# Optimization experiments

Measured on AMD Instinct MI355X. Metric: run time of the kernel, lower is better.

## Reference

```python
import jax, jax.numpy as jnp
import numpy as np

DIM = 1024
N_HEADS = 16
HEAD_DIM = DIM // N_HEADS
FF_DIM = 4096
EPS = 1e-8


def rms_norm(x, scale):
    # norm = ||x||_2 * d^{-1/2}; out = scale * x / (norm + eps)
    norm = jnp.linalg.norm(x, axis=-1, keepdims=True) * (x.shape[-1] ** -0.5)
    return scale * x / (norm + EPS)


def rope_cos_sin(seq_len, dtype=jnp.float32):
    # inv_freq over even indices of head_dim; after the truncation branch in
    # apply_rotary_pos_emb, effective cos/sin have size head_dim//2.
    inv_freq = 1.0 / (10000.0 ** (jnp.arange(0, HEAD_DIM, 2, dtype=jnp.float32) / HEAD_DIM))
    t = jnp.arange(seq_len, dtype=jnp.float32)
    freqs = t[:, None] * inv_freq[None, :]  # [S, head_dim//2]
    return jnp.cos(freqs).astype(dtype), jnp.sin(freqs).astype(dtype)


def apply_rope(x, cos, sin):
    # x: [B, S, H, hd]; cos/sin: [S, hd//2] broadcast over batch and heads
    c = cos[None, :, None, :]
    s = sin[None, :, None, :]
    x1, x2 = jnp.split(x, 2, axis=-1)
    return jnp.concatenate([x1 * c - x2 * s, x1 * s + x2 * c], axis=-1)


def setup_inputs() -> dict:
    key = jax.random.key(0)
    ks = jax.random.split(key, 10)
    B, S = 2, 2048
    std = DIM ** -0.5
    inp = {
        "x": jax.random.normal(ks[0], (B, S, DIM), jnp.float32),
        "mask": jnp.tril(jnp.ones((S, S), dtype=bool)),
        "qkv_w": jax.random.normal(ks[1], (3 * DIM, DIM), jnp.float32) * std,
        "attn_out_w": jax.random.normal(ks[2], (DIM, DIM), jnp.float32) * std,
        "gate_w": jax.random.normal(ks[3], (FF_DIM, DIM), jnp.float32) * std,
        "gate_b": jnp.zeros((FF_DIM,), jnp.float32),
        "lin_w": jax.random.normal(ks[4], (FF_DIM, DIM), jnp.float32) * std,
        "lin_b": jnp.zeros((FF_DIM,), jnp.float32),
        "ff_out_w": jax.random.normal(ks[5], (DIM, FF_DIM), jnp.float32) * (FF_DIM ** -0.5),
        "norm1_scale": jnp.ones((DIM,), jnp.float32),
        "norm2_scale": jnp.ones((DIM,), jnp.float32),
    }
    return inp


def reference(x, mask, qkv_w, attn_out_w, gate_w, gate_b, lin_w, lin_b,
              ff_out_w, norm1_scale, norm2_scale):
    B, S, _ = x.shape
    residual = x
    qkv = (x @ qkv_w.T).reshape(B, S, 3, N_HEADS, HEAD_DIM)
    q, k, v = qkv[:, :, 0], qkv[:, :, 1], qkv[:, :, 2]  # [B,S,H,hd]
    cos, sin = rope_cos_sin(S, x.dtype)
    q = apply_rope(q, cos, sin)
    k = apply_rope(k, cos, sin)
    # naive full attention, materializing [B,H,S,S] as the source does
    scores = jnp.einsum('bqhd,bkhd->bhqk', q, k) / jnp.sqrt(jnp.asarray(HEAD_DIM, x.dtype))
    scores = jnp.where(mask[None, None, :, :], scores, jnp.asarray(-1e9, x.dtype))
    attn = jax.nn.softmax(scores, axis=-1)
    out = jnp.einsum('bhqk,bkhd->bqhd', attn, v).reshape(B, S, DIM)
    out = out @ attn_out_w.T
    x = rms_norm(residual + out, norm1_scale)
    residual = x
    ff = jax.nn.sigmoid(x @ gate_w.T + gate_b) * (x @ lin_w.T + lin_b)
    ff = ff @ ff_out_w.T
    x = rms_norm(residual + ff, norm2_scale)
    return x
```

## Files before the change

kernel.cpp:

```cpp
#include <hip/hip_runtime.h>
#include <hip/hip_bf16.h>
#include <math.h>

#define DIMSZ 1024
#define NHEAD 16
#define HDIM 64
#define FFDIM 4096
#define SEQ 2048
#define NBATCH 2

typedef unsigned short ushortt;
typedef __attribute__((ext_vector_type(8))) short frag8;
typedef __attribute__((ext_vector_type(4))) float f32x4;

__device__ __forceinline__ float u2f(ushortt u) {
  return __uint_as_float(((unsigned)u) << 16);
}
__device__ __forceinline__ ushortt f2bu(float f) {
  unsigned x = __float_as_uint(f);
  return (ushortt)((x + 0x7FFFu + ((x >> 16) & 1u)) >> 16);
}

__global__ __launch_bounds__(256) void cast_f2b(
    const float* __restrict__ src, ushortt* __restrict__ dst, int n) {
  int i = (blockIdx.x * 256 + threadIdx.x) * 4;
  if (i >= n) return;
  float4 f = *(const float4*)(src + i);
  ushort4 u;
  u.x = f2bu(f.x); u.y = f2bu(f.y); u.z = f2bu(f.z); u.w = f2bu(f.w);
  *(ushort4*)(dst + i) = u;
}

template <int EPI>
__global__ __launch_bounds__(256) void gemm_mfma(
    const ushortt* __restrict__ A, const ushortt* __restrict__ W,
    void* __restrict__ Cv, int M, int N, int K) {
  __shared__ __align__(16) short As[2][128 * 32];
  __shared__ __align__(16) short Bs[2][128 * 32];
  const int tid = threadIdx.x;
  const int wave = tid >> 6;
  const int lane = tid & 63;
  const int bm = blockIdx.y * 128;
  const int bn = blockIdx.x * 128;
  const int wm = (wave >> 1) * 64;
  const int wn = (wave & 1) * 64;

  f32x4 acc[4][4] = {};

  const int sr = lane >> 2;
  const int sc = (lane & 3) * 8;
  const ushortt* pa0 = A + (size_t)(bm + wave * 16 + sr) * K + sc;
  const ushortt* pa1 = pa0 + (size_t)64 * K;
  const ushortt* pb0 = W + (size_t)(bn + wave * 16 + sr) * K + sc;
  const ushortt* pb1 = pb0 + (size_t)64 * K;
  const int lo0 = (wave * 16) * 32;
  const int lo1 = (64 + wave * 16) * 32;

  const int fr = lane & 15;
  const int fq = (lane >> 4) * 8;
  const int nt = K >> 5;

  auto stage = [&](int t, int buf) {
    const int ko = t * 32;
    short* ab = &As[0][0] + buf * 4096;
    short* bb = &Bs[0][0] + buf * 4096;
    __builtin_amdgcn_global_load_lds(
        (const __attribute__((address_space(1))) void*)(pa0 + ko),
        (__attribute__((address_space(3))) void*)(ab + lo0), 16, 0, 0);
    __builtin_amdgcn_global_load_lds(
        (const __attribute__((address_space(1))) void*)(pa1 + ko),
        (__attribute__((address_space(3))) void*)(ab + lo1), 16, 0, 0);
    __builtin_amdgcn_global_load_lds(
        (const __attribute__((address_space(1))) void*)(pb0 + ko),
        (__attribute__((address_space(3))) void*)(bb + lo0), 16, 0, 0);
    __builtin_amdgcn_global_load_lds(
        (const __attribute__((address_space(1))) void*)(pb1 + ko),
        (__attribute__((address_space(3))) void*)(bb + lo1), 16, 0, 0);
  };

  stage(0, 0);
  __syncthreads();

  for (int t = 0; t < nt; ++t) {
    if (t + 1 < nt) stage(t + 1, (t + 1) & 1);
    const short* as = &As[0][0] + (t & 1) * 4096;
    const short* bs = &Bs[0][0] + (t & 1) * 4096;

    frag8 af[4], bf[4];
#pragma unroll
    for (int mi = 0; mi < 4; ++mi)
      af[mi] = *(const frag8*)&as[(wm + mi * 16 + fr) * 32 + fq];
#pragma unroll
    for (int ni = 0; ni < 4; ++ni)
      bf[ni] = *(const frag8*)&bs[(wn + ni * 16 + fr) * 32 + fq];
#pragma unroll
    for (int mi = 0; mi < 4; ++mi)
#pragma unroll
      for (int ni = 0; ni < 4; ++ni)
        acc[mi][ni] = __builtin_amdgcn_mfma_f32_16x16x32_bf16(
            af[mi], bf[ni], acc[mi][ni], 0, 0, 0);
    __syncthreads();
  }

  const int er = (lane >> 4) * 4;
  const int ec = lane & 15;
#pragma unroll
  for (int mi = 0; mi < 4; ++mi)
#pragma unroll
    for (int ni = 0; ni < 4; ++ni)
#pragma unroll
      for (int r = 0; r < 4; ++r) {
        int m = bm + wm + mi * 16 + er + r;
        int n = bn + wn + ni * 16 + ec;
        size_t o = (size_t)m * N + n;
        float v = acc[mi][ni][r];
        if (EPI == 0) {
          ((float*)Cv)[o] = v;
        } else {
          ((ushortt*)Cv)[o] = f2bu(v);
        }
      }
}

__global__ __launch_bounds__(256) void gemm_gatelin(
    const ushortt* __restrict__ A, const ushortt* __restrict__ Wg,
    const ushortt* __restrict__ Wl, ushortt* __restrict__ Cv,
    const float* __restrict__ gbias, const float* __restrict__ lbias,
    int M, int N, int K) {
  __shared__ __align__(16) short As[2][128 * 32];
  __shared__ __align__(16) short Gs[2][128 * 32];
  __shared__ __align__(16) short Ls[2][128 * 32];
  const int tid = threadIdx.x;
  const int wave = tid >> 6;
  const int lane = tid & 63;
  const int bm = blockIdx.y * 128;
  const int bn = blockIdx.x * 128;
  const int wm = (wave >> 1) * 64;
  const int wn = (wave & 1) * 64;

  f32x4 accg[4][4] = {};
  f32x4 accl[4][4] = {};

  const int sr = lane >> 2;
  const int sc = (lane & 3) * 8;
  const ushortt* pa0 = A + (size_t)(bm + wave * 16 + sr) * K + sc;
  const ushortt* pa1 = pa0 + (size_t)64 * K;
  const ushortt* pg0 = Wg + (size_t)(bn + wave * 16 + sr) * K + sc;
  const ushortt* pg1 = pg0 + (size_t)64 * K;
  const ushortt* pl0 = Wl + (size_t)(bn + wave * 16 + sr) * K + sc;
  const ushortt* pl1 = pl0 + (size_t)64 * K;
  const int lo0 = (wave * 16) * 32;
  const int lo1 = (64 + wave * 16) * 32;

  const int fr = lane & 15;
  const int fq = (lane >> 4) * 8;
  const int nt = K >> 5;

  auto stage = [&](int t, int buf) {
    const int ko = t * 32;
    short* ab = &As[0][0] + buf * 4096;
    short* gb = &Gs[0][0] + buf * 4096;
    short* lb = &Ls[0][0] + buf * 4096;
    __builtin_amdgcn_global_load_lds(
        (const __attribute__((address_space(1))) void*)(pa0 + ko),
        (__attribute__((address_space(3))) void*)(ab + lo0), 16, 0, 0);
    __builtin_amdgcn_global_load_lds(
        (const __attribute__((address_space(1))) void*)(pa1 + ko),
        (__attribute__((address_space(3))) void*)(ab + lo1), 16, 0, 0);
    __builtin_amdgcn_global_load_lds(
        (const __attribute__((address_space(1))) void*)(pg0 + ko),
        (__attribute__((address_space(3))) void*)(gb + lo0), 16, 0, 0);
    __builtin_amdgcn_global_load_lds(
        (const __attribute__((address_space(1))) void*)(pg1 + ko),
        (__attribute__((address_space(3))) void*)(gb + lo1), 16, 0, 0);
    __builtin_amdgcn_global_load_lds(
        (const __attribute__((address_space(1))) void*)(pl0 + ko),
        (__attribute__((address_space(3))) void*)(lb + lo0), 16, 0, 0);
    __builtin_amdgcn_global_load_lds(
        (const __attribute__((address_space(1))) void*)(pl1 + ko),
        (__attribute__((address_space(3))) void*)(lb + lo1), 16, 0, 0);
  };

  stage(0, 0);
  __syncthreads();

  for (int t = 0; t < nt; ++t) {
    if (t + 1 < nt) stage(t + 1, (t + 1) & 1);
    const short* as = &As[0][0] + (t & 1) * 4096;
    const short* gs = &Gs[0][0] + (t & 1) * 4096;
    const short* ls = &Ls[0][0] + (t & 1) * 4096;

    frag8 af[4], gf[4], lf[4];
#pragma unroll
    for (int mi = 0; mi < 4; ++mi)
      af[mi] = *(const frag8*)&as[(wm + mi * 16 + fr) * 32 + fq];
#pragma unroll
    for (int ni = 0; ni < 4; ++ni) {
      gf[ni] = *(const frag8*)&gs[(wn + ni * 16 + fr) * 32 + fq];
      lf[ni] = *(const frag8*)&ls[(wn + ni * 16 + fr) * 32 + fq];
    }
#pragma unroll
    for (int mi = 0; mi < 4; ++mi)
#pragma unroll
      for (int ni = 0; ni < 4; ++ni) {
        accg[mi][ni] = __builtin_amdgcn_mfma_f32_16x16x32_bf16(
            af[mi], gf[ni], accg[mi][ni], 0, 0, 0);
        accl[mi][ni] = __builtin_amdgcn_mfma_f32_16x16x32_bf16(
            af[mi], lf[ni], accl[mi][ni], 0, 0, 0);
      }
    __syncthreads();
  }

  const int er = (lane >> 4) * 4;
  const int ec = lane & 15;
#pragma unroll
  for (int mi = 0; mi < 4; ++mi)
#pragma unroll
    for (int ni = 0; ni < 4; ++ni)
#pragma unroll
      for (int r = 0; r < 4; ++r) {
        int m = bm + wm + mi * 16 + er + r;
        int n = bn + wn + ni * 16 + ec;
        size_t o = (size_t)m * N + n;
        float g = accg[mi][ni][r] + gbias[n];
        float l = accl[mi][ni][r] + lbias[n];
        float sig = 1.0f / (1.0f + __expf(-g));
        ((ushortt*)Cv)[o] = f2bu(sig * l);
      }
}

__global__ __launch_bounds__(256) void gemm_ffout(
    const ushortt* __restrict__ A, const float* __restrict__ Bw,
    float* __restrict__ C, int lda, int koff, int first) {
  __shared__ __align__(16) short As[2][128 * 32];
  __shared__ __align__(16) short Bs[2][128 * 32];
  const int tid = threadIdx.x;
  const int wave = tid >> 6;
  const int lane = tid & 63;
  const int bm = blockIdx.y * 128;
  const int bn = blockIdx.x * 128;
  const int wm = (wave >> 1) * 64;
  const int wn = (wave & 1) * 64;

  f32x4 acc[4][4] = {};

  const int sr = lane >> 2;
  const int sc = (lane & 3) * 8;
  const ushortt* pa0 = A + (size_t)(bm + wave * 16 + sr) * lda + sc;
  const ushortt* pa1 = pa0 + (size_t)64 * lda;
  const int lo0 = (wave * 16) * 32;
  const int lo1 = (64 + wave * 16) * 32;

  const int br = tid >> 2;
  const int kc = (tid & 3) * 8;
  const float* pb0 = Bw + (size_t)(bn + br) * FFDIM + koff + kc;
  const float* pb1 = pb0 + (size_t)64 * FFDIM;

  const int fr = lane & 15;
  const int fq = (lane >> 4) * 8;
  const int nt = 2048 >> 5;

  float4 f0, f1, f2, f3;
  auto bload = [&](int t) {
    const float* p0 = pb0 + t * 32;
    const float* p1 = pb1 + t * 32;
    f0 = *(const float4*)p0; f1 = *(const float4*)(p0 + 4);
    f2 = *(const float4*)p1; f3 = *(const float4*)(p1 + 4);
  };
  auto pk = [&](float4 a, float4 b) {
    frag8 v;
    v[0] = (short)f2bu(a.x); v[1] = (short)f2bu(a.y);
    v[2] = (short)f2bu(a.z); v[3] = (short)f2bu(a.w);
    v[4] = (short)f2bu(b.x); v[5] = (short)f2bu(b.y);
    v[6] = (short)f2bu(b.z); v[7] = (short)f2bu(b.w);
    return v;
  };
  auto bwrite = [&](int buf) {
    *(frag8*)&Bs[buf][tid * 8] = pk(f0, f1);
    *(frag8*)&Bs[buf][2048 + tid * 8] = pk(f2, f3);
  };
  auto astage = [&](int t, int buf) {
    const int ko = t * 32;
    short* ab = &As[0][0] + buf * 4096;
    __builtin_amdgcn_global_load_lds(
        (const __attribute__((address_space(1))) void*)(pa0 + ko),
        (__attribute__((address_space(3))) void*)(ab + lo0), 16, 0, 0);
    __builtin_amdgcn_global_load_lds(
        (const __attribute__((address_space(1))) void*)(pa1 + ko),
        (__attribute__((address_space(3))) void*)(ab + lo1), 16, 0, 0);
  };

  astage(0, 0);
  bload(0);
  bwrite(0);
  __syncthreads();

  for (int t = 0; t < nt; ++t) {
    if (t + 1 < nt) {
      astage(t + 1, (t + 1) & 1);
      bload(t + 1);
    }
    const short* as = &As[0][0] + (t & 1) * 4096;
    const short* bs = &Bs[0][0] + (t & 1) * 4096;

    frag8 af[4], bf[4];
#pragma unroll
    for (int mi = 0; mi < 4; ++mi)
      af[mi] = *(const frag8*)&as[(wm + mi * 16 + fr) * 32 + fq];
#pragma unroll
    for (int ni = 0; ni < 4; ++ni)
      bf[ni] = *(const frag8*)&bs[(wn + ni * 16 + fr) * 32 + fq];
#pragma unroll
    for (int mi = 0; mi < 4; ++mi)
#pragma unroll
      for (int ni = 0; ni < 4; ++ni)
        acc[mi][ni] = __builtin_amdgcn_mfma_f32_16x16x32_bf16(
            af[mi], bf[ni], acc[mi][ni], 0, 0, 0);
    if (t + 1 < nt) bwrite((t + 1) & 1);
    __syncthreads();
  }

  const int er = (lane >> 4) * 4;
  const int ec = lane & 15;
#pragma unroll
  for (int mi = 0; mi < 4; ++mi)
#pragma unroll
    for (int ni = 0; ni < 4; ++ni)
#pragma unroll
      for (int r = 0; r < 4; ++r) {
        int m = bm + wm + mi * 16 + er + r;
        int n = bn + wn + ni * 16 + ec;
        size_t o = (size_t)m * 1024 + n;
        float v = acc[mi][ni][r];
        C[o] = first ? v : C[o] + v;
      }
}

__global__ __launch_bounds__(256) void rope_prep(
    const ushortt* __restrict__ qkv, ushortt* __restrict__ Qr,
    ushortt* __restrict__ Kr, ushortt* __restrict__ Vr) {
  const int s0 = blockIdx.x * 64;
  const int bh = blockIdx.y;
  const int b = bh >> 4, h = bh & 15;
  const int tid = threadIdx.x;
  __shared__ float ifr_s[32];
  __shared__ ushortt vt[64][72];
  if (tid < 32) ifr_s[tid] = __powf(10000.0f, -(float)tid * (1.0f / 32.0f));
  __syncthreads();
  const size_t qbase = (size_t)bh * SEQ * 64;

#pragma unroll
  for (int i = 0; i < 8; ++i) {
    int p = i * 256 + tid;
    int r = p >> 5, d = p & 31;
    size_t src = ((size_t)(b * SEQ + s0 + r)) * (3 * DIMSZ) + h * 64 + d;
    float q1 = u2f(qkv[src]), q2 = u2f(qkv[src + 32]);
    float k1 = u2f(qkv[src + DIMSZ]), k2 = u2f(qkv[src + DIMSZ + 32]);
    float ang = (float)(s0 + r) * ifr_s[d];
    float sn, cs;
    __sincosf(ang, &sn, &cs);
    size_t dst = qbase + (size_t)(s0 + r) * 64 + d;
    Qr[dst]      = f2bu((q1 * cs - q2 * sn) * 0.125f);
    Qr[dst + 32] = f2bu((q1 * sn + q2 * cs) * 0.125f);
    Kr[dst]      = f2bu(k1 * cs - k2 * sn);
    Kr[dst + 32] = f2bu(k1 * sn + k2 * cs);
  }

#pragma unroll
  for (int i = 0; i < 2; ++i) {
    int e = (i * 256 + tid) * 8;
    int r = e >> 6, d0 = e & 63;
    size_t src = ((size_t)(b * SEQ + s0 + r)) * (3 * DIMSZ) + 2 * DIMSZ + h * 64 + d0;
    *(ushort4*)&vt[r][d0]     = *(const ushort4*)(qkv + src);
    *(ushort4*)&vt[r][d0 + 4] = *(const ushort4*)(qkv + src + 4);
  }
  __syncthreads();
  {
    int d = tid >> 2;
    int sc0 = (tid & 3) * 16;
    size_t dst = (size_t)bh * 64 * SEQ + (size_t)blockIdx.x * 4096 +
                 (size_t)d * 64 + sc0;
    ushortt tmp[16];
#pragma unroll
    for (int j = 0; j < 16; ++j) tmp[j] = vt[sc0 + j][d];
    *(ushort4*)(Vr + dst)      = *(ushort4*)&tmp[0];
    *(ushort4*)(Vr + dst + 4)  = *(ushort4*)&tmp[4];
    *(ushort4*)(Vr + dst + 8)  = *(ushort4*)&tmp[8];
    *(ushort4*)(Vr + dst + 12) = *(ushort4*)&tmp[12];
  }
}

__global__ __launch_bounds__(512) void flash_mfma(
    const ushortt* __restrict__ Qr, const ushortt* __restrict__ Kr,
    const ushortt* __restrict__ Vr, ushortt* __restrict__ ctx) {
  const int id = blockIdx.x;
  const int r5 = id & 255;
  const int qt0 = r5 >> 5;
  const int qt = (id & 256) ? (15 - qt0) : qt0;
  const int bh = r5 & 31;
  const int q0 = qt * 128;
  const int b = bh >> 4, h = bh & 15;
  const int tid = threadIdx.x;
  const int w = tid >> 6;
  const int lane = tid & 63;
  const int fr = lane & 15;
  const int quad = lane >> 4;

  __shared__ __align__(16) short Kb[2][4096];
  __shared__ __align__(16) short Vb[2][4096];
  __shared__ __align__(16) ushortt Ps[8][16][72];

  const size_t qkbase = (size_t)bh * SEQ * 64;
  const size_t vbase = (size_t)bh * 64 * SEQ;

  const int lin = (w << 10) + ((lane & 63) << 4);
  const int swz = lin ^ (((lin >> 7) & 7) << 4);
  const char* ksrc = (const char*)(Kr + qkbase) + swz;
  const char* vsrc = (const char*)(Vr + vbase) + swz;
  short* kdst[2] = {&Kb[0][w * 512], &Kb[1][w * 512]};
  short* vdst[2] = {&Vb[0][w * 512], &Vb[1][w * 512]};

  frag8 aq[2];
#pragma unroll
  for (int hh = 0; hh < 2; ++hh)
    aq[hh] = *(const frag8*)(Qr + qkbase + (size_t)(q0 + w * 16 + fr) * 64 +
                             hh * 32 + quad * 8);

  float mr[4], lr[4];
  f32x4 od[4] = {};
#pragma unroll
  for (int r = 0; r < 4; ++r) { mr[r] = -1e30f; lr[r] = 0.0f; }

  const int nt = 2 * qt + 2;

  __builtin_amdgcn_global_load_lds(
      (const __attribute__((address_space(1))) void*)ksrc,
      (__attribute__((address_space(3))) void*)kdst[0], 16, 0, 0);
  __builtin_amdgcn_global_load_lds(
      (const __attribute__((address_space(1))) void*)vsrc,
      (__attribute__((address_space(3))) void*)vdst[0], 16, 0, 0);
  __syncthreads();

  for (int t = 0; t < nt; ++t) {
    const int c0 = t * 64;
    if (t + 1 < nt) {
      const char* kn = ksrc + (size_t)(t + 1) * 8192;
      const char* vn = vsrc + (size_t)(t + 1) * 8192;
      __builtin_amdgcn_global_load_lds(
          (const __attribute__((address_space(1))) void*)kn,
          (__attribute__((address_space(3))) void*)kdst[(t + 1) & 1], 16, 0, 0);
      __builtin_amdgcn_global_load_lds(
          (const __attribute__((address_space(1))) void*)vn,
          (__attribute__((address_space(3))) void*)vdst[(t + 1) & 1], 16, 0, 0);
    }
    const char* kcur = (const char*)Kb[t & 1];
    const char* vcur = (const char*)Vb[t & 1];

    if (c0 <= q0 + w * 16 + 15) {
      f32x4 sc[4] = {};
#pragma unroll
      for (int ni = 0; ni < 4; ++ni)
#pragma unroll
        for (int hh = 0; hh < 2; ++hh) {
          int kb = (((ni * 16 + fr) << 7) + (hh << 6) + (quad << 4)) ^
                   ((fr & 7) << 4);
          frag8 kf = *(const frag8*)(kcur + kb);
          sc[ni] = __builtin_amdgcn_mfma_f32_16x16x32_bf16(aq[hh], kf, sc[ni],
                                                           0, 0, 0);
        }

      if (c0 + 63 > q0 + w * 16) {
        int rowb = q0 + w * 16 + quad * 4;
#pragma unroll
        for (int ni = 0; ni < 4; ++ni) {
          int col = c0 + ni * 16 + fr;
#pragma unroll
          for (int r = 0; r < 4; ++r)
            if (col > rowb + r) sc[ni][r] = -1e30f;
        }
      }

#pragma unroll
      for (int r = 0; r < 4; ++r) {
        float cm = fmaxf(fmaxf(sc[0][r], sc[1][r]), fmaxf(sc[2][r], sc[3][r]));
        for (int off = 1; off < 16; off <<= 1)
          cm = fmaxf(cm, __shfl_xor(cm, off, 16));
        float mn = fmaxf(mr[r], cm);
        float corr = __expf(mr[r] - mn);
        mr[r] = mn;
        float ps = 0.0f;
#pragma unroll
        for (int ni = 0; ni < 4; ++ni) {
          float p = __expf(sc[ni][r] - mn);
          Ps[w][quad * 4 + r][ni * 16 + fr] = f2bu(p);
          ps += p;
        }
        for (int off = 1; off < 16; off <<= 1) ps += __shfl_xor(ps, off, 16);
        lr[r] = lr[r] * corr + ps;
#pragma unroll
        for (int dt = 0; dt < 4; ++dt) od[dt][r] *= corr;
      }

      frag8 pf[2];
#pragma unroll
      for (int hh = 0; hh < 2; ++hh)
        pf[hh] = *(const frag8*)&Ps[w][fr][hh * 32 + quad * 8];
#pragma unroll
      for (int dt = 0; dt < 4; ++dt)
#pragma unroll
        for (int hh = 0; hh < 2; ++hh) {
          int vb_ = (((dt * 16 + fr) << 7) + (hh << 6) + (quad << 4)) ^
                    ((fr & 7) << 4);
          frag8 vf = *(const frag8*)(vcur + vb_);
          od[dt] = __builtin_amdgcn_mfma_f32_16x16x32_bf16(pf[hh], vf, od[dt],
                                                           0, 0, 0);
        }
    }
    __syncthreads();
  }

#pragma unroll
  for (int r = 0; r < 4; ++r) {
    float inv = 1.0f / lr[r];
    size_t row = (size_t)(b * SEQ + q0 + w * 16 + quad * 4 + r) * DIMSZ + h * 64;
#pragma unroll
    for (int dt = 0; dt < 4; ++dt)
      ctx[row + dt * 16 + fr] = f2bu(od[dt][r] * inv);
  }
}

template <int DUAL>
__global__ __launch_bounds__(256) void add_rmsnorm(
    const float* __restrict__ res, const float* __restrict__ proj,
    const float* __restrict__ scale, float* __restrict__ out,
    ushortt* __restrict__ out2) {
  const int row = blockIdx.x;
  const int tid = threadIdx.x;
  const size_t base = (size_t)row * DIMSZ;
  __shared__ float red[4];
  float y[4];
  float ss = 0.0f;
#pragma unroll
  for (int j = 0; j < 4; ++j) {
    int d = tid + j * 256;
    float yv = res[base + d] + proj[base + d];
    y[j] = yv;
    ss += yv * yv;
  }
  for (int off = 1; off < 64; off <<= 1) ss += __shfl_xor(ss, off, 64);
  if ((tid & 63) == 0) red[tid >> 6] = ss;
  __syncthreads();
  float tot = red[0] + red[1] + red[2] + red[3];
  float norm = sqrtf(tot) * 0.03125f;
  float inv = 1.0f / (norm + 1e-8f);
#pragma unroll
  for (int j = 0; j < 4; ++j) {
    int d = tid + j * 256;
    float v = scale[d] * y[j] * inv;
    out[base + d] = v;
    if (DUAL) out2[base + d] = f2bu(v);
  }
}

extern "C" void kernel_launch(void* const* d_in, const int* in_sizes, int n_in,
                              void* d_out, int out_size, void* d_ws, size_t ws_size,
                              hipStream_t stream) {
  const float* x          = (const float*)d_in[0];
  const float* qkv_w      = (const float*)d_in[2];
  const float* attn_out_w = (const float*)d_in[3];
  const float* gate_w     = (const float*)d_in[4];
  const float* gate_b     = (const float*)d_in[5];
  const float* lin_w      = (const float*)d_in[6];
  const float* lin_b      = (const float*)d_in[7];
  const float* ff_out_w   = (const float*)d_in[8];
  const float* n1s        = (const float*)d_in[9];
  const float* n2s        = (const float*)d_in[10];
  float* out = (float*)d_out;

  const int M = NBATCH * SEQ;
  char* ws = (char*)d_ws;
  char* dob = (char*)d_out;
  const size_t MB = 1 << 20;
  ushortt* qkv_tmp = (ushortt*)(ws + 0);
  ushortt* xb      = (ushortt*)(ws + 24 * MB);
  ushortt* qkv_wb  = (ushortt*)(ws + 32 * MB);
  ushortt* Qr      = (ushortt*)(ws + 24 * MB);
  ushortt* Kr      = (ushortt*)(ws + 32 * MB);
  ushortt* Vr      = (ushortt*)(ws + 40 * MB);
  ushortt* attn_wb = (ushortt*)(ws + 24 * MB);
  float*   proj    = (float*)(ws + 0);
  float*   x1      = (float*)(ws + 16 * MB);
  ushortt* x1b     = (ushortt*)(ws + 32 * MB);
  float*   proj2   = (float*)(ws + 0);
  ushortt* gcb     = (ushortt*)(ws + 40 * MB);
  ushortt* lcb     = (ushortt*)(ws + 44 * MB);
  ushortt* ctx  = (ushortt*)(dob + 0);
  ushortt* ffc  = (ushortt*)(dob + 0);

  cast_f2b<<<4194304 / 1024, 256, 0, stream>>>(x, xb, 4194304);
  cast_f2b<<<3145728 / 1024, 256, 0, stream>>>(qkv_w, qkv_wb, 3145728);
  gemm_mfma<1><<<dim3(3072 / 128, M / 128), 256, 0, stream>>>(
      xb, qkv_wb, qkv_tmp, M, 3072, DIMSZ);
  rope_prep<<<dim3(SEQ / 64, NBATCH * NHEAD), 256, 0, stream>>>(
      qkv_tmp, Qr, Kr, Vr);
  flash_mfma<<<(SEQ / 128) * NBATCH * NHEAD, 512, 0, stream>>>(
      Qr, Kr, Vr, ctx);
  cast_f2b<<<1048576 / 1024, 256, 0, stream>>>(attn_out_w, attn_wb, 1048576);
  gemm_mfma<0><<<dim3(DIMSZ / 128, M / 128), 256, 0, stream>>>(
      ctx, attn_wb, proj, M, DIMSZ, DIMSZ);
  add_rmsnorm<1><<<M, 256, 0, stream>>>(x, proj, n1s, x1, x1b);
  for (int c = 0; c < 2; ++c) {
    cast_f2b<<<2048, 256, 0, stream>>>(
        gate_w + (size_t)c * 2097152, gcb, 2097152);
    cast_f2b<<<2048, 256, 0, stream>>>(
        lin_w + (size_t)c * 2097152, lcb, 2097152);
    gemm_gatelin<<<dim3(2048 / 128, M / 128), 256, 0, stream>>>(
        x1b, gcb, lcb, ffc, gate_b + c * 2048, lin_b + c * 2048,
        M, 2048, DIMSZ);
    gemm_ffout<<<dim3(1024 / 128, M / 128), 256, 0, stream>>>(
        ffc, ff_out_w, proj2, 2048, c * 2048, c == 0 ? 1 : 0);
  }
  add_rmsnorm<0><<<M, 256, 0, stream>>>(x1, proj2, n2s, out, nullptr);
}
```

Baseline: 607.5 us.

## Add split-K atomics, XCD-aware tile mapping, and fuse fp32 weight casts into gatelin

```diff
diff --git a/kernel.cpp b/kernel.cpp
--- a/kernel.cpp
+++ b/kernel.cpp
@@ -31,17 +31,25 @@
   *(ushort4*)(dst + i) = u;
 }
 
-template <int EPI>
+__global__ __launch_bounds__(256) void zero_f32(float* __restrict__ p, int n) {
+  int i = (blockIdx.x * 256 + threadIdx.x) * 4;
+  if (i < n) *(float4*)(p + i) = make_float4(0.f, 0.f, 0.f, 0.f);
+}
+
+template <int EPI, int SK>
 __global__ __launch_bounds__(256) void gemm_mfma(
     const ushortt* __restrict__ A, const ushortt* __restrict__ W,
-    void* __restrict__ Cv, int M, int N, int K) {
+    void* __restrict__ Cv, int M, int N, int K, int KB) {
   __shared__ __align__(16) short As[2][128 * 32];
   __shared__ __align__(16) short Bs[2][128 * 32];
   const int tid = threadIdx.x;
   const int wave = tid >> 6;
   const int lane = tid & 63;
-  const int bm = blockIdx.y * 128;
-  const int bn = blockIdx.x * 128;
+  int xcd = blockIdx.x & 7, r = blockIdx.x >> 3, kz = 0;
+  if (SK == 2) { kz = r & 1; r >>= 1; }
+  const int bm = (xcd * 4 + (r & 3)) * 128;
+  const int bn = (r >> 2) * 128;
+  const int ko0 = kz * KB;
   const int wm = (wave >> 1) * 64;
   const int wn = (wave & 1) * 64;
 
@@ -49,16 +57,16 @@
 
   const int sr = lane >> 2;
   const int sc = (lane & 3) * 8;
-  const ushortt* pa0 = A + (size_t)(bm + wave * 16 + sr) * K + sc;
+  const ushortt* pa0 = A + (size_t)(bm + wave * 16 + sr) * K + ko0 + sc;
   const ushortt* pa1 = pa0 + (size_t)64 * K;
-  const ushortt* pb0 = W + (size_t)(bn + wave * 16 + sr) * K + sc;
+  const ushortt* pb0 = W + (size_t)(bn + wave * 16 + sr) * K + ko0 + sc;
   const ushortt* pb1 = pb0 + (size_t)64 * K;
   const int lo0 = (wave * 16) * 32;
   const int lo1 = (64 + wave * 16) * 32;
 
   const int fr = lane & 15;
   const int fq = (lane >> 4) * 8;
-  const int nt = K >> 5;
+  const int nt = KB >> 5;
 
   auto stage = [&](int t, int buf) {
     const int ko = t * 32;
@@ -109,22 +117,24 @@
 #pragma unroll
     for (int ni = 0; ni < 4; ++ni)
 #pragma unroll
-      for (int r = 0; r < 4; ++r) {
-        int m = bm + wm + mi * 16 + er + r;
+      for (int r2 = 0; r2 < 4; ++r2) {
+        int m = bm + wm + mi * 16 + er + r2;
         int n = bn + wn + ni * 16 + ec;
         size_t o = (size_t)m * N + n;
-        float v = acc[mi][ni][r];
+        float v = acc[mi][ni][r2];
         if (EPI == 0) {
           ((float*)Cv)[o] = v;
+        } else if (EPI == 1) {
+          ((ushortt*)Cv)[o] = f2bu(v);
         } else {
-          ((ushortt*)Cv)[o] = f2bu(v);
+          unsafeAtomicAdd((float*)Cv + o, v);
         }
       }
 }
 
 __global__ __launch_bounds__(256) void gemm_gatelin(
-    const ushortt* __restrict__ A, const ushortt* __restrict__ Wg,
-    const ushortt* __restrict__ Wl, ushortt* __restrict__ Cv,
+    const ushortt* __restrict__ A, const float* __restrict__ Wg,
+    const float* __restrict__ Wl, ushortt* __restrict__ Cv,
     const float* __restrict__ gbias, const float* __restrict__ lbias,
     int M, int N, int K) {
   __shared__ __align__(16) short As[2][128 * 32];
@@ -133,8 +143,9 @@
   const int tid = threadIdx.x;
   const int wave = tid >> 6;
   const int lane = tid & 63;
-  const int bm = blockIdx.y * 128;
-  const int bn = blockIdx.x * 128;
+  int xcd = blockIdx.x & 7, r = blockIdx.x >> 3;
+  const int bm = (xcd * 4 + (r & 3)) * 128;
+  const int bn = (r >> 2) * 128;
   const int wm = (wave >> 1) * 64;
   const int wn = (wave & 1) * 64;
 
@@ -145,127 +156,26 @@
   const int sc = (lane & 3) * 8;
   const ushortt* pa0 = A + (size_t)(bm + wave * 16 + sr) * K + sc;
   const ushortt* pa1 = pa0 + (size_t)64 * K;
-  const ushortt* pg0 = Wg + (size_t)(bn + wave * 16 + sr) * K + sc;
-  const ushortt* pg1 = pg0 + (size_t)64 * K;
-  const ushortt* pl0 = Wl + (size_t)(bn + wave * 16 + sr) * K + sc;
-  const ushortt* pl1 = pl0 + (size_t)64 * K;
   const int lo0 = (wave * 16) * 32;
   const int lo1 = (64 + wave * 16) * 32;
+
+  const int br = tid >> 2;
+  const int kc = (tid & 3) * 8;
+  const float* pg = Wg + (size_t)(bn + br) * DIMSZ + kc;
+  const float* pl = Wl + (size_t)(bn + br) * DIMSZ + kc;
 
   const int fr = lane & 15;
   const int fq = (lane >> 4) * 8;
   const int nt = K >> 5;
 
-  auto stage = [&](int t, int buf) {
-    const int ko = t * 32;
-    short* ab = &As[0][0] + buf * 4096;
-    short* gb = &Gs[0][0] + buf * 4096;
-    short* lb = &Ls[0][0] + buf * 4096;
-    __builtin_amdgcn_global_load_lds(
-        (const __attribute__((address_space(1))) void*)(pa0 + ko),
-        (__attribute__((address_space(3))) void*)(ab + lo0), 16, 0, 0);
-    __builtin_amdgcn_global_load_lds(
-        (const __attribute__((address_space(1))) void*)(pa1 + ko),
-        (__attribute__((address_space(3))) void*)(ab + lo1), 16, 0, 0);
-    __builtin_amdgcn_global_load_lds(
-        (const __attribute__((address_space(1))) void*)(pg0 + ko),
-        (__attribute__((address_space(3))) void*)(gb + lo0), 16, 0, 0);
-    __builtin_amdgcn_global_load_lds(
-        (const __attribute__((address_space(1))) void*)(pg1 + ko),
-        (__attribute__((address_space(3))) void*)(gb + lo1), 16, 0, 0);
-    __builtin_amdgcn_global_load_lds(
-        (const __attribute__((address_space(1))) void*)(pl0 + ko),
-        (__attribute__((address_space(3))) void*)(lb + lo0), 16, 0, 0);
-    __builtin_amdgcn_global_load_lds(
-        (const __attribute__((address_space(1))) void*)(pl1 + ko),
-        (__attribute__((address_space(3))) void*)(lb + lo1), 16, 0, 0);
-  };
-
-  stage(0, 0);
-  __syncthreads();
-
-  for (int t = 0; t < nt; ++t) {
-    if (t + 1 < nt) stage(t + 1, (t + 1) & 1);
-    const short* as = &As[0][0] + (t & 1) * 4096;
-    const short* gs = &Gs[0][0] + (t & 1) * 4096;
-    const short* ls = &Ls[0][0] + (t & 1) * 4096;
-
-    frag8 af[4], gf[4], lf[4];
-#pragma unroll
-    for (int mi = 0; mi < 4; ++mi)
-      af[mi] = *(const frag8*)&as[(wm + mi * 16 + fr) * 32 + fq];
-#pragma unroll
-    for (int ni = 0; ni < 4; ++ni) {
-      gf[ni] = *(const frag8*)&gs[(wn + ni * 16 + fr) * 32 + fq];
-      lf[ni] = *(const frag8*)&ls[(wn + ni * 16 + fr) * 32 + fq];
-    }
-#pragma unroll
-    for (int mi = 0; mi < 4; ++mi)
-#pragma unroll
-      for (int ni = 0; ni < 4; ++ni) {
-        accg[mi][ni] = __builtin_amdgcn_mfma_f32_16x16x32_bf16(
-            af[mi], gf[ni], accg[mi][ni], 0, 0, 0);
-        accl[mi][ni] = __builtin_amdgcn_mfma_f32_16x16x32_bf16(
-            af[mi], lf[ni], accl[mi][ni], 0, 0, 0);
-      }
-    __syncthreads();
-  }
-
-  const int er = (lane >> 4) * 4;
-  const int ec = lane & 15;
-#pragma unroll
-  for (int mi = 0; mi < 4; ++mi)
-#pragma unroll
-    for (int ni = 0; ni < 4; ++ni)
-#pragma unroll
-      for (int r = 0; r < 4; ++r) {
-        int m = bm + wm + mi * 16 + er + r;
-        int n = bn + wn + ni * 16 + ec;
-        size_t o = (size_t)m * N + n;
-        float g = accg[mi][ni][r] + gbias[n];
-        float l = accl[mi][ni][r] + lbias[n];
-        float sig = 1.0f / (1.0f + __expf(-g));
-        ((ushortt*)Cv)[o] = f2bu(sig * l);
-      }
-}
-
-__global__ __launch_bounds__(256) void gemm_ffout(
-    const ushortt* __restrict__ A, const float* __restrict__ Bw,
-    float* __restrict__ C, int lda, int koff, int first) {
-  __shared__ __align__(16) short As[2][128 * 32];
-  __shared__ __align__(16) short Bs[2][128 * 32];
-  const int tid = threadIdx.x;
-  const int wave = tid >> 6;
-  const int lane = tid & 63;
-  const int bm = blockIdx.y * 128;
-  const int bn = blockIdx.x * 128;
-  const int wm = (wave >> 1) * 64;
-  const int wn = (wave & 1) * 64;
-
-  f32x4 acc[4][4] = {};
-
-  const int sr = lane >> 2;
-  const int sc = (lane & 3) * 8;
-  const ushortt* pa0 = A + (size_t)(bm + wave * 16 + sr) * lda + sc;
-  const ushortt* pa1 = pa0 + (size_t)64 * lda;
-  const int lo0 = (wave * 16) * 32;
-  const int lo1 = (64 + wave * 16) * 32;
-
-  const int br = tid >> 2;
-  const int kc = (tid & 3) * 8;
-  const float* pb0 = Bw + (size_t)(bn + br) * FFDIM + koff + kc;
-  const float* pb1 = pb0 + (size_t)64 * FFDIM;
-
-  const int fr = lane & 15;
-  const int fq = (lane >> 4) * 8;
-  const int nt = 2048 >> 5;
-
-  float4 f0, f1, f2, f3;
+  float4 g0, g1, g2, g3, l0, l1, l2, l3;
   auto bload = [&](int t) {
-    const float* p0 = pb0 + t * 32;
-    const float* p1 = pb1 + t * 32;
-    f0 = *(const float4*)p0; f1 = *(const float4*)(p0 + 4);
-    f2 = *(const float4*)p1; f3 = *(const float4*)(p1 + 4);
+    const float* p = pg + t * 32;
+    g0 = *(const float4*)p; g1 = *(const float4*)(p + 4);
+    g2 = *(const float4*)(p + 64 * DIMSZ); g3 = *(const float4*)(p + 64 * DIMSZ + 4);
+    const float* q = pl + t * 32;
+    l0 = *(const float4*)q; l1 = *(const float4*)(q + 4);
+    l2 = *(const float4*)(q + 64 * DIMSZ); l3 = *(const float4*)(q + 64 * DIMSZ + 4);
   };
   auto pk = [&](float4 a, float4 b) {
     frag8 v;
@@ -276,6 +186,125 @@
     return v;
   };
   auto bwrite = [&](int buf) {
+    *(frag8*)&Gs[buf][tid * 8] = pk(g0, g1);
+    *(frag8*)&Gs[buf][2048 + tid * 8] = pk(g2, g3);
+    *(frag8*)&Ls[buf][tid * 8] = pk(l0, l1);
+    *(frag8*)&Ls[buf][2048 + tid * 8] = pk(l2, l3);
+  };
+  auto astage = [&](int t, int buf) {
+    const int ko = t * 32;
+    short* ab = &As[0][0] + buf * 4096;
+    __builtin_amdgcn_global_load_lds(
+        (const __attribute__((address_space(1))) void*)(pa0 + ko),
+        (__attribute__((address_space(3))) void*)(ab + lo0), 16, 0, 0);
+    __builtin_amdgcn_global_load_lds(
+        (const __attribute__((address_space(1))) void*)(pa1 + ko),
+        (__attribute__((address_space(3))) void*)(ab + lo1), 16, 0, 0);
+  };
+
+  astage(0, 0);
+  bload(0);
+  bwrite(0);
+  __syncthreads();
+
+  for (int t = 0; t < nt; ++t) {
+    if (t + 1 < nt) {
+      astage(t + 1, (t + 1) & 1);
+      bload(t + 1);
+    }
+    const short* as = &As[0][0] + (t & 1) * 4096;
+    const short* gs = &Gs[0][0] + (t & 1) * 4096;
+    const short* ls = &Ls[0][0] + (t & 1) * 4096;
+
+    frag8 af[4], gf[4], lf[4];
+#pragma unroll
+    for (int mi = 0; mi < 4; ++mi)
+      af[mi] = *(const frag8*)&as[(wm + mi * 16 + fr) * 32 + fq];
+#pragma unroll
+    for (int ni = 0; ni < 4; ++ni) {
+      gf[ni] = *(const frag8*)&gs[(wn + ni * 16 + fr) * 32 + fq];
+      lf[ni] = *(const frag8*)&ls[(wn + ni * 16 + fr) * 32 + fq];
+    }
+#pragma unroll
+    for (int mi = 0; mi < 4; ++mi)
+#pragma unroll
+      for (int ni = 0; ni < 4; ++ni) {
+        accg[mi][ni] = __builtin_amdgcn_mfma_f32_16x16x32_bf16(
+            af[mi], gf[ni], accg[mi][ni], 0, 0, 0);
+        accl[mi][ni] = __builtin_amdgcn_mfma_f32_16x16x32_bf16(
+            af[mi], lf[ni], accl[mi][ni], 0, 0, 0);
+      }
+    if (t + 1 < nt) bwrite((t + 1) & 1);
+    __syncthreads();
+  }
+
+  const int er = (lane >> 4) * 4;
+  const int ec = lane & 15;
+#pragma unroll
+  for (int mi = 0; mi < 4; ++mi)
+#pragma unroll
+    for (int ni = 0; ni < 4; ++ni)
+#pragma unroll
+      for (int r2 = 0; r2 < 4; ++r2) {
+        int m = bm + wm + mi * 16 + er + r2;
+        int n = bn + wn + ni * 16 + ec;
+        size_t o = (size_t)m * N + n;
+        float g = accg[mi][ni][r2] + gbias[n];
+        float l = accl[mi][ni][r2] + lbias[n];
+        float sig = 1.0f / (1.0f + __expf(-g));
+        ((ushortt*)Cv)[o] = f2bu(sig * l);
+      }
+}
+
+__global__ __launch_bounds__(256) void gemm_ffout(
+    const ushortt* __restrict__ A, const float* __restrict__ Bw,
+    float* __restrict__ C, int koff) {
+  __shared__ __align__(16) short As[2][128 * 32];
+  __shared__ __align__(16) short Bs[2][128 * 32];
+  const int tid = threadIdx.x;
+  const int wave = tid >> 6;
+  const int lane = tid & 63;
+  int xcd = blockIdx.x & 7, r = blockIdx.x >> 3;
+  const int kz = r & 1; r >>= 1;
+  const int bm = (xcd * 4 + (r & 3)) * 128;
+  const int bn = (r >> 2) * 128;
+  const int wm = (wave >> 1) * 64;
+  const int wn = (wave & 1) * 64;
+
+  f32x4 acc[4][4] = {};
+
+  const int sr = lane >> 2;
+  const int sc = (lane & 3) * 8;
+  const ushortt* pa0 = A + (size_t)(bm + wave * 16 + sr) * 2048 + kz * 1024 + sc;
+  const ushortt* pa1 = pa0 + (size_t)64 * 2048;
+  const int lo0 = (wave * 16) * 32;
+  const int lo1 = (64 + wave * 16) * 32;
+
+  const int br = tid >> 2;
+  const int kc = (tid & 3) * 8;
+  const float* pb0 = Bw + (size_t)(bn + br) * FFDIM + koff + kz * 1024 + kc;
+  const float* pb1 = pb0 + (size_t)64 * FFDIM;
+
+  const int fr = lane & 15;
+  const int fq = (lane >> 4) * 8;
+  const int nt = 1024 >> 5;
+
+  float4 f0, f1, f2, f3;
+  auto bload = [&](int t) {
+    const float* p0 = pb0 + t * 32;
+    const float* p1 = pb1 + t * 32;
+    f0 = *(const float4*)p0; f1 = *(const float4*)(p0 + 4);
+    f2 = *(const float4*)p1; f3 = *(const float4*)(p1 + 4);
+  };
+  auto pk = [&](float4 a, float4 b) {
+    frag8 v;
+    v[0] = (short)f2bu(a.x); v[1] = (short)f2bu(a.y);
+    v[2] = (short)f2bu(a.z); v[3] = (short)f2bu(a.w);
+    v[4] = (short)f2bu(b.x); v[5] = (short)f2bu(b.y);
+    v[6] = (short)f2bu(b.z); v[7] = (short)f2bu(b.w);
+    return v;
+  };
+  auto bwrite = [&](int buf) {
     *(frag8*)&Bs[buf][tid * 8] = pk(f0, f1);
     *(frag8*)&Bs[buf][2048 + tid * 8] = pk(f2, f3);
   };
@@ -327,12 +356,10 @@
 #pragma unroll
     for (int ni = 0; ni < 4; ++ni)
 #pragma unroll
-      for (int r = 0; r < 4; ++r) {
-        int m = bm + wm + mi * 16 + er + r;
+      for (int r2 = 0; r2 < 4; ++r2) {
+        int m = bm + wm + mi * 16 + er + r2;
         int n = bn + wn + ni * 16 + ec;
-        size_t o = (size_t)m * 1024 + n;
-        float v = acc[mi][ni][r];
-        C[o] = first ? v : C[o] + v;
+        unsafeAtomicAdd(C + (size_t)m * 1024 + n, acc[mi][ni][r2]);
       }
 }
 
@@ -592,33 +619,29 @@
   float*   x1      = (float*)(ws + 16 * MB);
   ushortt* x1b     = (ushortt*)(ws + 32 * MB);
   float*   proj2   = (float*)(ws + 0);
-  ushortt* gcb     = (ushortt*)(ws + 40 * MB);
-  ushortt* lcb     = (ushortt*)(ws + 44 * MB);
   ushortt* ctx  = (ushortt*)(dob + 0);
   ushortt* ffc  = (ushortt*)(dob + 0);
 
   cast_f2b<<<4194304 / 1024, 256, 0, stream>>>(x, xb, 4194304);
   cast_f2b<<<3145728 / 1024, 256, 0, stream>>>(qkv_w, qkv_wb, 3145728);
-  gemm_mfma<1><<<dim3(3072 / 128, M / 128), 256, 0, stream>>>(
-      xb, qkv_wb, qkv_tmp, M, 3072, DIMSZ);
+  gemm_mfma<1, 1><<<(3072 / 128) * 32, 256, 0, stream>>>(
+      xb, qkv_wb, qkv_tmp, M, 3072, DIMSZ, DIMSZ);
   rope_prep<<<dim3(SEQ / 64, NBATCH * NHEAD), 256, 0, stream>>>(
       qkv_tmp, Qr, Kr, Vr);
   flash_mfma<<<(SEQ / 128) * NBATCH * NHEAD, 512, 0, stream>>>(
       Qr, Kr, Vr, ctx);
   cast_f2b<<<1048576 / 1024, 256, 0, stream>>>(attn_out_w, attn_wb, 1048576);
-  gemm_mfma<0><<<dim3(DIMSZ / 128, M / 128), 256, 0, stream>>>(
-      ctx, attn_wb, proj, M, DIMSZ, DIMSZ);
+  zero_f32<<<4194304 / 1024, 256, 0, stream>>>(proj, 4194304);
+  gemm_mfma<2, 2><<<(DIMSZ / 128) * 32 * 2, 256, 0, stream>>>(
+      ctx, attn_wb, proj, M, DIMSZ, DIMSZ, 512);
   add_rmsnorm<1><<<M, 256, 0, stream>>>(x, proj, n1s, x1, x1b);
+  zero_f32<<<4194304 / 1024, 256, 0, stream>>>(proj2, 4194304);
   for (int c = 0; c < 2; ++c) {
-    cast_f2b<<<2048, 256, 0, stream>>>(
-        gate_w + (size_t)c * 2097152, gcb, 2097152);
-    cast_f2b<<<2048, 256, 0, stream>>>(
-        lin_w + (size_t)c * 2097152, lcb, 2097152);
-    gemm_gatelin<<<dim3(2048 / 128, M / 128), 256, 0, stream>>>(
-        x1b, gcb, lcb, ffc, gate_b + c * 2048, lin_b + c * 2048,
-        M, 2048, DIMSZ);
-    gemm_ffout<<<dim3(1024 / 128, M / 128), 256, 0, stream>>>(
-        ffc, ff_out_w, proj2, 2048, c * 2048, c == 0 ? 1 : 0);
+    gemm_gatelin<<<(2048 / 128) * 32, 256, 0, stream>>>(
+        x1b, gate_w + (size_t)c * 2097152, lin_w + (size_t)c * 2097152,
+        ffc, gate_b + c * 2048, lin_b + c * 2048, M, 2048, DIMSZ);
+    gemm_ffout<<<(1024 / 128) * 32 * 2, 256, 0, stream>>>(
+        ffc, ff_out_w, proj2, c * 2048);
   }
   add_rmsnorm<0><<<M, 256, 0, stream>>>(x1, proj2, n2s, out, nullptr);
 }
```

Result: slower. 659.5 us (+8.6%).

## Remap GEMM tiles per XCD and split-K small GEMMs with atomics

Applied to the files above, without the earlier changes.

```diff
diff --git a/kernel.cpp b/kernel.cpp
--- a/kernel.cpp
+++ b/kernel.cpp
@@ -31,17 +31,25 @@
   *(ushort4*)(dst + i) = u;
 }
 
-template <int EPI>
+__global__ __launch_bounds__(256) void zero_f32(float* __restrict__ p, int n) {
+  int i = (blockIdx.x * 256 + threadIdx.x) * 4;
+  if (i < n) *(float4*)(p + i) = make_float4(0.f, 0.f, 0.f, 0.f);
+}
+
+template <int EPI, int SK>
 __global__ __launch_bounds__(256) void gemm_mfma(
     const ushortt* __restrict__ A, const ushortt* __restrict__ W,
-    void* __restrict__ Cv, int M, int N, int K) {
+    void* __restrict__ Cv, int M, int N, int K, int KB, size_t skoff) {
   __shared__ __align__(16) short As[2][128 * 32];
   __shared__ __align__(16) short Bs[2][128 * 32];
   const int tid = threadIdx.x;
   const int wave = tid >> 6;
   const int lane = tid & 63;
-  const int bm = blockIdx.y * 128;
-  const int bn = blockIdx.x * 128;
+  int xcd = blockIdx.x & 7, r = blockIdx.x >> 3, kz = 0;
+  if (SK == 2) { kz = r & 1; r >>= 1; }
+  const int bm = (xcd * 4 + (r & 3)) * 128;
+  const int bn = (r >> 2) * 128;
+  const int ko0 = kz * KB;
   const int wm = (wave >> 1) * 64;
   const int wn = (wave & 1) * 64;
 
@@ -49,16 +57,16 @@
 
   const int sr = lane >> 2;
   const int sc = (lane & 3) * 8;
-  const ushortt* pa0 = A + (size_t)(bm + wave * 16 + sr) * K + sc;
+  const ushortt* pa0 = A + (size_t)(bm + wave * 16 + sr) * K + ko0 + sc;
   const ushortt* pa1 = pa0 + (size_t)64 * K;
-  const ushortt* pb0 = W + (size_t)(bn + wave * 16 + sr) * K + sc;
+  const ushortt* pb0 = W + (size_t)(bn + wave * 16 + sr) * K + ko0 + sc;
   const ushortt* pb1 = pb0 + (size_t)64 * K;
   const int lo0 = (wave * 16) * 32;
   const int lo1 = (64 + wave * 16) * 32;
 
   const int fr = lane & 15;
   const int fq = (lane >> 4) * 8;
-  const int nt = K >> 5;
+  const int nt = KB >> 5;
 
   auto stage = [&](int t, int buf) {
     const int ko = t * 32;
@@ -104,18 +112,19 @@
 
   const int er = (lane >> 4) * 4;
   const int ec = lane & 15;
+  float* C0 = (float*)Cv + (SK == 2 ? (size_t)kz * skoff : 0);
 #pragma unroll
   for (int mi = 0; mi < 4; ++mi)
 #pragma unroll
     for (int ni = 0; ni < 4; ++ni)
 #pragma unroll
-      for (int r = 0; r < 4; ++r) {
-        int m = bm + wm + mi * 16 + er + r;
+      for (int r2 = 0; r2 < 4; ++r2) {
+        int m = bm + wm + mi * 16 + er + r2;
         int n = bn + wn + ni * 16 + ec;
         size_t o = (size_t)m * N + n;
-        float v = acc[mi][ni][r];
+        float v = acc[mi][ni][r2];
         if (EPI == 0) {
-          ((float*)Cv)[o] = v;
+          C0[o] = v;
         } else {
           ((ushortt*)Cv)[o] = f2bu(v);
         }
@@ -133,8 +142,9 @@
   const int tid = threadIdx.x;
   const int wave = tid >> 6;
   const int lane = tid & 63;
-  const int bm = blockIdx.y * 128;
-  const int bn = blockIdx.x * 128;
+  int xcd = blockIdx.x & 7, r = blockIdx.x >> 3;
+  const int bm = (xcd * 4 + (r & 3)) * 128;
+  const int bn = (r >> 2) * 128;
   const int wm = (wave >> 1) * 64;
   const int wn = (wave & 1) * 64;
 
@@ -218,12 +228,12 @@
 #pragma unroll
     for (int ni = 0; ni < 4; ++ni)
 #pragma unroll
-      for (int r = 0; r < 4; ++r) {
-        int m = bm + wm + mi * 16 + er + r;
+      for (int r2 = 0; r2 < 4; ++r2) {
+        int m = bm + wm + mi * 16 + er + r2;
         int n = bn + wn + ni * 16 + ec;
         size_t o = (size_t)m * N + n;
-        float g = accg[mi][ni][r] + gbias[n];
-        float l = accl[mi][ni][r] + lbias[n];
+        float g = accg[mi][ni][r2] + gbias[n];
+        float l = accl[mi][ni][r2] + lbias[n];
         float sig = 1.0f / (1.0f + __expf(-g));
         ((ushortt*)Cv)[o] = f2bu(sig * l);
       }
@@ -231,14 +241,16 @@
 
 __global__ __launch_bounds__(256) void gemm_ffout(
     const ushortt* __restrict__ A, const float* __restrict__ Bw,
-    float* __restrict__ C, int lda, int koff, int first) {
+    float* __restrict__ C, int koff) {
   __shared__ __align__(16) short As[2][128 * 32];
   __shared__ __align__(16) short Bs[2][128 * 32];
   const int tid = threadIdx.x;
   const int wave = tid >> 6;
   const int lane = tid & 63;
-  const int bm = blockIdx.y * 128;
-  const int bn = blockIdx.x * 128;
+  int xcd = blockIdx.x & 7, r = blockIdx.x >> 3;
+  const int kz = r & 1; r >>= 1;
+  const int bm = (xcd * 4 + (r & 3)) * 128;
+  const int bn = (r >> 2) * 128;
   const int wm = (wave >> 1) * 64;
   const int wn = (wave & 1) * 64;
 
@@ -246,19 +258,19 @@
 
   const int sr = lane >> 2;
   const int sc = (lane & 3) * 8;
-  const ushortt* pa0 = A + (size_t)(bm + wave * 16 + sr) * lda + sc;
-  const ushortt* pa1 = pa0 + (size_t)64 * lda;
+  const ushortt* pa0 = A + (size_t)(bm + wave * 16 + sr) * 2048 + kz * 1024 + sc;
+  const ushortt* pa1 = pa0 + (size_t)64 * 2048;
   const int lo0 = (wave * 16) * 32;
   const int lo1 = (64 + wave * 16) * 32;
 
   const int br = tid >> 2;
   const int kc = (tid & 3) * 8;
-  const float* pb0 = Bw + (size_t)(bn + br) * FFDIM + koff + kc;
+  const float* pb0 = Bw + (size_t)(bn + br) * FFDIM + koff + kz * 1024 + kc;
   const float* pb1 = pb0 + (size_t)64 * FFDIM;
 
   const int fr = lane & 15;
   const int fq = (lane >> 4) * 8;
-  const int nt = 2048 >> 5;
+  const int nt = 1024 >> 5;
 
   float4 f0, f1, f2, f3;
   auto bload = [&](int t) {
@@ -327,12 +339,10 @@
 #pragma unroll
     for (int ni = 0; ni < 4; ++ni)
 #pragma unroll
-      for (int r = 0; r < 4; ++r) {
-        int m = bm + wm + mi * 16 + er + r;
+      for (int r2 = 0; r2 < 4; ++r2) {
+        int m = bm + wm + mi * 16 + er + r2;
         int n = bn + wn + ni * 16 + ec;
-        size_t o = (size_t)m * 1024 + n;
-        float v = acc[mi][ni][r];
-        C[o] = first ? v : C[o] + v;
+        unsafeAtomicAdd(C + (size_t)m * 1024 + n, acc[mi][ni][r2]);
       }
 }
 
@@ -529,11 +539,11 @@
   }
 }
 
-template <int DUAL>
+template <int DUAL, int NP>
 __global__ __launch_bounds__(256) void add_rmsnorm(
-    const float* __restrict__ res, const float* __restrict__ proj,
-    const float* __restrict__ scale, float* __restrict__ out,
-    ushortt* __restrict__ out2) {
+    const float* __restrict__ res, const float* __restrict__ pa,
+    const float* __restrict__ pb, const float* __restrict__ scale,
+    float* __restrict__ out, ushortt* __restrict__ out2) {
   const int row = blockIdx.x;
   const int tid = threadIdx.x;
   const size_t base = (size_t)row * DIMSZ;
@@ -543,7 +553,8 @@
 #pragma unroll
   for (int j = 0; j < 4; ++j) {
     int d = tid + j * 256;
-    float yv = res[base + d] + proj[base + d];
+    float yv = res[base + d] + pa[base + d];
+    if (NP == 3) yv += pb[base + d];
     y[j] = yv;
     ss += yv * yv;
   }
@@ -588,7 +599,8 @@
   ushortt* Kr      = (ushortt*)(ws + 32 * MB);
   ushortt* Vr      = (ushortt*)(ws + 40 * MB);
   ushortt* attn_wb = (ushortt*)(ws + 24 * MB);
-  float*   proj    = (float*)(ws + 0);
+  float*   proj_a  = (float*)(ws + 0);
+  float*   proj_b  = (float*)(ws + 40 * MB);
   float*   x1      = (float*)(ws + 16 * MB);
   ushortt* x1b     = (ushortt*)(ws + 32 * MB);
   float*   proj2   = (float*)(ws + 0);
@@ -599,26 +611,29 @@
 
   cast_f2b<<<4194304 / 1024, 256, 0, stream>>>(x, xb, 4194304);
   cast_f2b<<<3145728 / 1024, 256, 0, stream>>>(qkv_w, qkv_wb, 3145728);
-  gemm_mfma<1><<<dim3(3072 / 128, M / 128), 256, 0, stream>>>(
-      xb, qkv_wb, qkv_tmp, M, 3072, DIMSZ);
+  gemm_mfma<1, 1><<<(3072 / 128) * 32, 256, 0, stream>>>(
+      xb, qkv_wb, qkv_tmp, M, 3072, DIMSZ, DIMSZ, 0);
   rope_prep<<<dim3(SEQ / 64, NBATCH * NHEAD), 256, 0, stream>>>(
       qkv_tmp, Qr, Kr, Vr);
   flash_mfma<<<(SEQ / 128) * NBATCH * NHEAD, 512, 0, stream>>>(
       Qr, Kr, Vr, ctx);
   cast_f2b<<<1048576 / 1024, 256, 0, stream>>>(attn_out_w, attn_wb, 1048576);
-  gemm_mfma<0><<<dim3(DIMSZ / 128, M / 128), 256, 0, stream>>>(
-      ctx, attn_wb, proj, M, DIMSZ, DIMSZ);
-  add_rmsnorm<1><<<M, 256, 0, stream>>>(x, proj, n1s, x1, x1b);
+  gemm_mfma<0, 2><<<(DIMSZ / 128) * 32 * 2, 256, 0, stream>>>(
+      ctx, attn_wb, proj_a, M, DIMSZ, DIMSZ, 512,
+      (size_t)(40 * MB) / sizeof(float));
+  add_rmsnorm<1, 3><<<M, 256, 0, stream>>>(x, proj_a, proj_b, n1s, x1, x1b);
+  zero_f32<<<4194304 / 1024, 256, 0, stream>>>(proj2, 4194304);
   for (int c = 0; c < 2; ++c) {
     cast_f2b<<<2048, 256, 0, stream>>>(
         gate_w + (size_t)c * 2097152, gcb, 2097152);
     cast_f2b<<<2048, 256, 0, stream>>>(
         lin_w + (size_t)c * 2097152, lcb, 2097152);
-    gemm_gatelin<<<dim3(2048 / 128, M / 128), 256, 0, stream>>>(
+    gemm_gatelin<<<(2048 / 128) * 32, 256, 0, stream>>>(
         x1b, gcb, lcb, ffc, gate_b + c * 2048, lin_b + c * 2048,
         M, 2048, DIMSZ);
-    gemm_ffout<<<dim3(1024 / 128, M / 128), 256, 0, stream>>>(
-        ffc, ff_out_w, proj2, 2048, c * 2048, c == 0 ? 1 : 0);
-  }
-  add_rmsnorm<0><<<M, 256, 0, stream>>>(x1, proj2, n2s, out, nullptr);
-}
+    gemm_ffout<<<(1024 / 128) * 32 * 2, 256, 0, stream>>>(
+        ffc, ff_out_w, proj2, c * 2048);
+  }
+  add_rmsnorm<0, 2><<<M, 256, 0, stream>>>(x1, proj2, nullptr, n2s, out,
+                                           nullptr);
+}
```

Result: faster. 563.9 us (-7.2%).
